# Performance work log

Measured on AMD Instinct MI355X. Metric: run time of the kernel, lower is better.

## Reference

```python
import jax, jax.numpy as jnp
import numpy as np

N_NODES = 100000
N_EDGES = 1600000
IN_DIM = 128
HID_DIM = 128


def gcn_conv(x, src, dst, W, b, n_nodes):
    """PyG GCNConv: out = D^{-1/2}(A+I)D^{-1/2} (x @ W) + b.
    src/dst already include self-loops."""
    h = x @ W  # [N, out_dim]
    deg = jnp.zeros((n_nodes,), dtype=h.dtype).at[dst].add(1.0)
    dis = jnp.where(deg > 0, jax.lax.rsqrt(jnp.maximum(deg, 1.0)), 0.0)
    norm = dis[src] * dis[dst]  # [E]
    msg = h[src] * norm[:, None]  # gather + scale, [E, out_dim]
    out = jax.ops.segment_sum(msg, dst, num_segments=n_nodes)
    return out + b


def setup_inputs() -> dict:
    key = jax.random.key(0)
    k1, k2, k3, k4, k5, k6 = jax.random.split(key, 6)
    x = jax.random.normal(k1, (N_NODES, IN_DIM), dtype=jnp.float32)
    edge_index = jax.random.randint(k2, (2, N_EDGES), 0, N_NODES, dtype=jnp.int32)
    s1 = 1.0 / np.sqrt(IN_DIM)
    s2 = 1.0 / np.sqrt(HID_DIM)
    W1 = jax.random.uniform(k3, (IN_DIM, HID_DIM), jnp.float32, -s1, s1)
    b1 = jax.random.uniform(k4, (HID_DIM,), jnp.float32, -s1, s1)
    W2 = jax.random.uniform(k5, (HID_DIM, HID_DIM), jnp.float32, -s2, s2)
    b2 = jax.random.uniform(k6, (HID_DIM,), jnp.float32, -s2, s2)
    return {"x": x, "edge_index": edge_index, "W1": W1, "b1": b1, "W2": W2, "b2": b2}


def reference(x, edge_index, W1, b1, W2, b2):
    n = x.shape[0]
    loops = jnp.arange(n, dtype=edge_index.dtype)
    src = jnp.concatenate([edge_index[0], loops])
    dst = jnp.concatenate([edge_index[1], loops])
    h = jax.nn.relu(gcn_conv(x, src, dst, W1, b1, n))
    h = jax.nn.relu(gcn_conv(h, src, dst, W2, b2, n))
    # global_mean_pool with batch = arange(N): each node is its own graph,
    # so the per-graph mean is the node feature itself.
    counts = jnp.ones((n, 1), dtype=h.dtype)
    pooled = jax.ops.segment_sum(h, jnp.arange(n), num_segments=n) / counts
    return pooled
```

## Files before the change

### kernel.cpp

```cpp
#include <hip/hip_runtime.h>
#include <hip/hip_fp16.h>
#include <stdint.h>
#include <stddef.h>

#define FEAT 128
#define BKT_SHIFT 8
#define TILE 4096
#define MAXB 400
#define CAP 4608

typedef _Float16 half8 __attribute__((ext_vector_type(8)));
typedef float f32x4 __attribute__((ext_vector_type(4)));


__global__ __launch_bounds__(256) void k_initB(int* __restrict__ cursorPad, int* __restrict__ allocCtr,
                                               const float* __restrict__ W1, const float* __restrict__ W2,
                                               _Float16* __restrict__ Wt1, _Float16* __restrict__ Wt2) {
  int i = blockIdx.x * 256 + threadIdx.x;
  if (i < MAXB * 16) cursorPad[i] = 0;
  if (i == 0) allocCtr[0] = 0;
  if (i < 32768) {
    int which = i >> 14, rem = i & 16383;
    int k = rem >> 7, nn = rem & 127;
    (which ? Wt2 : Wt1)[nn * 128 + k] = (_Float16)((which ? W2 : W1)[rem]);
  }
}


__global__ __launch_bounds__(256) void k_bscatter(const int* __restrict__ src, const int* __restrict__ dst,
                                                  int* __restrict__ cursorPad, int* __restrict__ pairs,
                                                  int E, int B) {
  __shared__ int h[MAXB];
  __shared__ int cur[MAXB];
  int t0 = blockIdx.x * TILE;
  int end = min(E, t0 + TILE);
  for (int i = threadIdx.x; i < B; i += 256) h[i] = 0;
  __syncthreads();
  if (end - t0 == TILE) {
    int d[16];
#pragma unroll
    for (int k = 0; k < 16; ++k) {
      d[k] = dst[t0 + threadIdx.x + k * 256];
      atomicAdd(&h[d[k] >> BKT_SHIFT], 1);
    }
    __syncthreads();
    for (int i = threadIdx.x; i < B; i += 256)
      cur[i] = h[i] ? atomicAdd(&cursorPad[i * 16], h[i]) : 0;
    __syncthreads();
#pragma unroll
    for (int k = 0; k < 16; ++k) {
      int e = t0 + threadIdx.x + k * 256;
      int b = d[k] >> BKT_SHIFT;
      int pos = atomicAdd(&cur[b], 1);
      if (pos < CAP) pairs[b * CAP + pos] = (src[e] << 8) | (d[k] & 255);
    }
  } else {
    for (int e = t0 + threadIdx.x; e < end; e += 256) atomicAdd(&h[dst[e] >> BKT_SHIFT], 1);
    __syncthreads();
    for (int i = threadIdx.x; i < B; i += 256)
      cur[i] = h[i] ? atomicAdd(&cursorPad[i * 16], h[i]) : 0;
    __syncthreads();
    for (int e = t0 + threadIdx.x; e < end; e += 256) {
      int dd = dst[e];
      int b = dd >> BKT_SHIFT;
      int pos = atomicAdd(&cur[b], 1);
      if (pos < CAP) pairs[b * CAP + pos] = (src[e] << 8) | (dd & 255);
    }
  }
}


__global__ __launch_bounds__(256) void k_csr(const int* __restrict__ pairs, const int* __restrict__ cursorPad,
                                             int* __restrict__ cnt, int* __restrict__ rowstart,
                                             float* __restrict__ dis, int* __restrict__ allocCtr,
                                             int* __restrict__ adj, int n) {
  __shared__ int deg[256];
  __shared__ int scan[256];
  __shared__ int curs[256];
  __shared__ int base;
  int b = blockIdx.x, t = threadIdx.x;
  int nodeBase = b << BKT_SHIFT;
  int e0 = b * CAP;
  int ecnt = min(cursorPad[b * 16], CAP);
  deg[t] = 0;
  __syncthreads();
  for (int i = t; i < ecnt; i += 256) atomicAdd(&deg[pairs[e0 + i] & 255], 1);
  __syncthreads();
  int d = deg[t];
  int padded = (d + 3) & ~3;
  scan[t] = padded;
  __syncthreads();
  for (int off = 1; off < 256; off <<= 1) {
    int x = scan[t];
    int y = (t >= off) ? scan[t - off] : 0;
    __syncthreads();
    scan[t] = x + y;
    __syncthreads();
  }
  int excl = scan[t] - padded;
  if (t == 255) base = atomicAdd(allocCtr, scan[t]);
  __syncthreads();
  int rs = base + excl;
  int node = nodeBase + t;
  if (node < n) {
    rowstart[node] = rs;
    cnt[node] = d;
    dis[node] = rsqrtf((float)(d + 1));
  }
  curs[t] = rs;
  __syncthreads();
  for (int i = t; i < ecnt; i += 256) {
    int pk = pairs[e0 + i];
    int pos = atomicAdd(&curs[pk & 255], 1);
    adj[pos] = pk >> 8;
  }
}


__global__ __launch_bounds__(256) void k_conv(const float* __restrict__ x, const float* __restrict__ dis,
                                              __half* __restrict__ t, int nElem) {
  int base = (blockIdx.x * 256 + threadIdx.x) * 4;
  if (base + 4 <= nElem) {
    float di = dis[base >> 7];
    float4 v = *(const float4*)(x + base);
    __half2* o = (__half2*)(t + base);
    o[0] = __floats2half2_rn(di * v.x, di * v.y);
    o[1] = __floats2half2_rn(di * v.z, di * v.w);
  }
}


__global__ __launch_bounds__(256) void k_agg(const __half* __restrict__ t, __half* __restrict__ z,
                                             const int* __restrict__ adj, const int* __restrict__ rowstart,
                                             const int* __restrict__ cnt, const float* __restrict__ dis, int n) {
  int node = blockIdx.x * 4 + (threadIdx.x >> 6);
  if (node >= n) return;
  int lane = threadIdx.x & 63;
  int rs = rowstart[node];
  int d = cnt[node];
  float di = dis[node];
  float2 a = __half22float2(((const __half2*)(t + (size_t)node * FEAT))[lane]);
  float ax = a.x, ay = a.y;
  int p = rs, e = rs + d;
#pragma unroll 2
  for (; p + 4 <= e; p += 4) {
    int4 j4 = *(const int4*)(adj + p);
    float2 h0 = __half22float2(((const __half2*)(t + (size_t)j4.x * FEAT))[lane]);
    float2 h1 = __half22float2(((const __half2*)(t + (size_t)j4.y * FEAT))[lane]);
    float2 h2 = __half22float2(((const __half2*)(t + (size_t)j4.z * FEAT))[lane]);
    float2 h3 = __half22float2(((const __half2*)(t + (size_t)j4.w * FEAT))[lane]);
    ax += (h0.x + h1.x) + (h2.x + h3.x);
    ay += (h0.y + h1.y) + (h2.y + h3.y);
  }
  for (; p < e; ++p) {
    int j = adj[p];
    float2 hv = __half22float2(((const __half2*)(t + (size_t)j * FEAT))[lane]);
    ax += hv.x; ay += hv.y;
  }
  ((__half2*)(z + (size_t)node * FEAT))[lane] = __floats2half2_rn(di * ax, di * ay);
}


template <bool OUT_HALF>
__global__ __launch_bounds__(256, 2) void k_gemm(const __half* __restrict__ Z,
                                                 const _Float16* __restrict__ Wt,
                                                 const float* __restrict__ bias,
                                                 const float* __restrict__ dis,
                                                 void* __restrict__ OutV, int n, int nwaves) {
  const int wid = (blockIdx.x * 256 + threadIdx.x) >> 6;
  const int lane = threadIdx.x & 63;
  const int lrow = lane & 15;
  const int lk8 = (lane >> 4) * 8;
  const int ngroups = (n + 15) >> 4;

  half8 bf[8][4];
#pragma unroll
  for (int c = 0; c < 8; ++c)
#pragma unroll
    for (int kk = 0; kk < 4; ++kk)
      bf[c][kk] = *(const half8*)(Wt + (size_t)(c * 16 + lrow) * 128 + kk * 32 + lk8);
  float bb[8];
#pragma unroll
  for (int c = 0; c < 8; ++c) bb[c] = bias[c * 16 + lrow];

  for (int g = wid; g < ngroups; g += nwaves) {
    int ar = g * 16 + lrow; if (ar >= n) ar = n - 1;
    const _Float16* arow = (const _Float16*)Z + (size_t)ar * 128 + lk8;
    half8 af[4];
#pragma unroll
    for (int kk = 0; kk < 4; ++kk) af[kk] = *(const half8*)(arow + kk * 32);
    f32x4 acc[8];
#pragma unroll
    for (int c = 0; c < 8; ++c) acc[c] = (f32x4){0.f, 0.f, 0.f, 0.f};
#pragma unroll
    for (int kk = 0; kk < 4; ++kk)
#pragma unroll
      for (int c = 0; c < 8; ++c)
        acc[c] = __builtin_amdgcn_mfma_f32_16x16x32_f16(af[kk], bf[c][kk], acc[c], 0, 0, 0);
    const int r0 = g * 16 + (lane >> 4) * 4;
#pragma unroll
    for (int r = 0; r < 4; ++r) {
      int row = r0 + r;
      if (row < n) {
        float sc = OUT_HALF ? dis[row] : 1.f;
#pragma unroll
        for (int c = 0; c < 8; ++c) {
          float vv = fmaxf(acc[c][r] + bb[c], 0.f);
          if (OUT_HALF) ((__half*)OutV)[(size_t)row * 128 + c * 16 + lrow] = __float2half_rn(sc * vv);
          else          ((float*)OutV)[(size_t)row * 128 + c * 16 + lrow] = vv;
        }
      }
    }
  }
}


extern "C" void kernel_launch(void* const* d_in, const int* in_sizes, int n_in,
                              void* d_out, int out_size, void* d_ws, size_t ws_size,
                              hipStream_t stream) {
  const float* x  = (const float*)d_in[0];
  const int*   ei = (const int*)d_in[1];
  const float* W1 = (const float*)d_in[2];
  const float* b1 = (const float*)d_in[3];
  const float* W2 = (const float*)d_in[4];
  const float* b2 = (const float*)d_in[5];
  float* out = (float*)d_out;

  const int n = in_sizes[0] / FEAT;
  const int E = in_sizes[1] / 2;
  const int B = (n + 255) >> BKT_SHIFT;
  const int* srcv = ei;
  const int* dstv = ei + E;

  uintptr_t p = (uintptr_t)d_ws;
  auto balloc = [&](size_t bytes) -> void* {
    void* r = (void*)p;
    p += (bytes + 255) & ~(size_t)255;
    return r;
  };
  __half*    T0   = (__half*)   balloc((size_t)n * FEAT * sizeof(__half));
  __half*    T1   = (__half*)   balloc((size_t)n * FEAT * sizeof(__half));
  __half*    Z16  = (__half*)   balloc((size_t)n * FEAT * sizeof(__half));
  _Float16*  Wt1  = (_Float16*) balloc(128 * 128 * sizeof(_Float16));
  _Float16*  Wt2  = (_Float16*) balloc(128 * 128 * sizeof(_Float16));
  int*   cnt      = (int*)  balloc((size_t)n * sizeof(int));
  int*   rowstart = (int*)  balloc((size_t)n * sizeof(int));
  float* dis      = (float*)balloc((size_t)n * sizeof(float));
  int*   allocCtr = (int*)  balloc(256);
  int*   cursorPad= (int*)  balloc((size_t)MAXB * 16 * sizeof(int));
  int*   pairs    = (int*)  balloc((size_t)MAXB * CAP * sizeof(int));
  int*   adj      = (int*)  balloc(((size_t)E + 4 * (size_t)n) * sizeof(int));
  (void)ws_size; (void)n_in; (void)out_size;

  const int nb  = (n + 255) / 256;
  const int tb  = (E + TILE - 1) / TILE;
  const int cb  = (n * FEAT / 4 + 255) / 256;

  k_initB   <<<nb, 256, 0, stream>>>(cursorPad, allocCtr, W1, W2, Wt1, Wt2);
  k_bscatter<<<tb, 256, 0, stream>>>(srcv, dstv, cursorPad, pairs, E, B);
  k_csr     <<<B, 256, 0, stream>>>(pairs, cursorPad, cnt, rowstart, dis, allocCtr, adj, n);
  k_conv    <<<cb, 256, 0, stream>>>(x, dis, T0, n * FEAT);

  const int ab = (n + 3) / 4;
  const int gemmBlocks = 512;
  const int nwaves = gemmBlocks * 4;

  k_agg        <<<ab, 256, 0, stream>>>(T0, Z16, adj, rowstart, cnt, dis, n);
  k_gemm<true> <<<gemmBlocks, 256, 0, stream>>>(Z16, Wt1, b1, dis, T1, n, nwaves);

  k_agg        <<<ab, 256, 0, stream>>>(T1, Z16, adj, rowstart, cnt, dis, n);
  k_gemm<false><<<gemmBlocks, 256, 0, stream>>>(Z16, Wt2, b2, dis, out, n, nwaves);
}
```

Measured before the change: 228.3 us.

## Fuse aggregation with GEMM via LDS tile and fold x conversion into CSR

The x-to-half scaling is folded into the CSR-building kernel, using the per-bucket degree values held in shared memory. Each layer's gather-aggregate is fused with the 128x128 MFMA GEMM: a block aggregates 16 nodes into a swizzled LDS tile, then its four waves each compute two output column groups. This removes the Z16 intermediate round trip and two kernel launches. In exchange, weight fragments are reloaded per block instead of staying in registers, and the CSR kernel now does extra streaming work in only about 400 blocks.

```diff
diff --git a/kernel.cpp b/kernel.cpp
--- a/kernel.cpp
+++ b/kernel.cpp
@@ -70,13 +70,15 @@
 }
 
 
-__global__ __launch_bounds__(256) void k_csr(const int* __restrict__ pairs, const int* __restrict__ cursorPad,
-                                             int* __restrict__ cnt, int* __restrict__ rowstart,
-                                             float* __restrict__ dis, int* __restrict__ allocCtr,
-                                             int* __restrict__ adj, int n) {
+__global__ __launch_bounds__(256) void k_csrc(const int* __restrict__ pairs, const int* __restrict__ cursorPad,
+                                              int* __restrict__ cnt, int* __restrict__ rowstart,
+                                              float* __restrict__ dis, int* __restrict__ allocCtr,
+                                              int* __restrict__ adj,
+                                              const float* __restrict__ x, __half* __restrict__ T0, int n) {
   __shared__ int deg[256];
   __shared__ int scan[256];
   __shared__ int curs[256];
+  __shared__ float disS[256];
   __shared__ int base;
   int b = blockIdx.x, t = threadIdx.x;
   int nodeBase = b << BKT_SHIFT;
@@ -91,10 +93,10 @@
   scan[t] = padded;
   __syncthreads();
   for (int off = 1; off < 256; off <<= 1) {
-    int x = scan[t];
+    int xg = scan[t];
     int y = (t >= off) ? scan[t - off] : 0;
     __syncthreads();
-    scan[t] = x + y;
+    scan[t] = xg + y;
     __syncthreads();
   }
   int excl = scan[t] - padded;
@@ -102,10 +104,12 @@
   __syncthreads();
   int rs = base + excl;
   int node = nodeBase + t;
+  float dv = rsqrtf((float)(d + 1));
+  disS[t] = dv;
   if (node < n) {
     rowstart[node] = rs;
     cnt[node] = d;
-    dis[node] = rsqrtf((float)(d + 1));
+    dis[node] = dv;
   }
   curs[t] = rs;
   __syncthreads();
@@ -114,101 +118,89 @@
     int pos = atomicAdd(&curs[pk & 255], 1);
     adj[pos] = pk >> 8;
   }
-}
-
-
-__global__ __launch_bounds__(256) void k_conv(const float* __restrict__ x, const float* __restrict__ dis,
-                                              __half* __restrict__ t, int nElem) {
-  int base = (blockIdx.x * 256 + threadIdx.x) * 4;
-  if (base + 4 <= nElem) {
-    float di = dis[base >> 7];
-    float4 v = *(const float4*)(x + base);
-    __half2* o = (__half2*)(t + base);
-    o[0] = __floats2half2_rn(di * v.x, di * v.y);
-    o[1] = __floats2half2_rn(di * v.z, di * v.w);
-  }
-}
-
-
-__global__ __launch_bounds__(256) void k_agg(const __half* __restrict__ t, __half* __restrict__ z,
-                                             const int* __restrict__ adj, const int* __restrict__ rowstart,
-                                             const int* __restrict__ cnt, const float* __restrict__ dis, int n) {
-  int node = blockIdx.x * 4 + (threadIdx.x >> 6);
-  if (node >= n) return;
-  int lane = threadIdx.x & 63;
-  int rs = rowstart[node];
-  int d = cnt[node];
-  float di = dis[node];
-  float2 a = __half22float2(((const __half2*)(t + (size_t)node * FEAT))[lane]);
-  float ax = a.x, ay = a.y;
-  int p = rs, e = rs + d;
+  for (int idx = t; idx < 256 * 32; idx += 256) {
+    int r = idx >> 5, c = idx & 31;
+    int nd = nodeBase + r;
+    if (nd >= n) continue;
+    float di = disS[r];
+    float4 v = ((const float4*)(x + (size_t)nd * FEAT))[c];
+    __half2 h0 = __floats2half2_rn(di * v.x, di * v.y);
+    __half2 h1 = __floats2half2_rn(di * v.z, di * v.w);
+    *(__half2*)(T0 + (size_t)nd * FEAT + c * 4)     = h0;
+    *(__half2*)(T0 + (size_t)nd * FEAT + c * 4 + 2) = h1;
+  }
+}
+
+
+template <bool OUT_HALF>
+__global__ __launch_bounds__(256) void k_fused(const __half* __restrict__ t, const _Float16* __restrict__ Wt,
+                                               const float* __restrict__ bias, const float* __restrict__ dis,
+                                               void* __restrict__ OutV,
+                                               const int* __restrict__ adj, const int* __restrict__ rowstart,
+                                               const int* __restrict__ cnt, int n) {
+  __shared__ __align__(16) char zb[16 * 256];
+  __shared__ float disL[16];
+  const int tid = threadIdx.x, w = tid >> 6, lane = tid & 63;
+  const int blockBase = blockIdx.x * 16;
+
+  for (int r = 0; r < 4; ++r) {
+    int local = w * 4 + r;
+    int node = blockBase + local;
+    float ax = 0.f, ay = 0.f, di = 0.f;
+    if (node < n) {
+      int rs = rowstart[node];
+      int d = cnt[node];
+      di = dis[node];
+      float2 a = __half22float2(((const __half2*)(t + (size_t)node * FEAT))[lane]);
+      ax = a.x; ay = a.y;
+      int p = rs, e = rs + d;
 #pragma unroll 2
-  for (; p + 4 <= e; p += 4) {
-    int4 j4 = *(const int4*)(adj + p);
-    float2 h0 = __half22float2(((const __half2*)(t + (size_t)j4.x * FEAT))[lane]);
-    float2 h1 = __half22float2(((const __half2*)(t + (size_t)j4.y * FEAT))[lane]);
-    float2 h2 = __half22float2(((const __half2*)(t + (size_t)j4.z * FEAT))[lane]);
-    float2 h3 = __half22float2(((const __half2*)(t + (size_t)j4.w * FEAT))[lane]);
-    ax += (h0.x + h1.x) + (h2.x + h3.x);
-    ay += (h0.y + h1.y) + (h2.y + h3.y);
-  }
-  for (; p < e; ++p) {
-    int j = adj[p];
-    float2 hv = __half22float2(((const __half2*)(t + (size_t)j * FEAT))[lane]);
-    ax += hv.x; ay += hv.y;
-  }
-  ((__half2*)(z + (size_t)node * FEAT))[lane] = __floats2half2_rn(di * ax, di * ay);
-}
-
-
-template <bool OUT_HALF>
-__global__ __launch_bounds__(256, 2) void k_gemm(const __half* __restrict__ Z,
-                                                 const _Float16* __restrict__ Wt,
-                                                 const float* __restrict__ bias,
-                                                 const float* __restrict__ dis,
-                                                 void* __restrict__ OutV, int n, int nwaves) {
-  const int wid = (blockIdx.x * 256 + threadIdx.x) >> 6;
-  const int lane = threadIdx.x & 63;
-  const int lrow = lane & 15;
-  const int lk8 = (lane >> 4) * 8;
-  const int ngroups = (n + 15) >> 4;
-
-  half8 bf[8][4];
-#pragma unroll
-  for (int c = 0; c < 8; ++c)
-#pragma unroll
-    for (int kk = 0; kk < 4; ++kk)
-      bf[c][kk] = *(const half8*)(Wt + (size_t)(c * 16 + lrow) * 128 + kk * 32 + lk8);
-  float bb[8];
-#pragma unroll
-  for (int c = 0; c < 8; ++c) bb[c] = bias[c * 16 + lrow];
-
-  for (int g = wid; g < ngroups; g += nwaves) {
-    int ar = g * 16 + lrow; if (ar >= n) ar = n - 1;
-    const _Float16* arow = (const _Float16*)Z + (size_t)ar * 128 + lk8;
-    half8 af[4];
-#pragma unroll
-    for (int kk = 0; kk < 4; ++kk) af[kk] = *(const half8*)(arow + kk * 32);
-    f32x4 acc[8];
-#pragma unroll
-    for (int c = 0; c < 8; ++c) acc[c] = (f32x4){0.f, 0.f, 0.f, 0.f};
-#pragma unroll
-    for (int kk = 0; kk < 4; ++kk)
-#pragma unroll
-      for (int c = 0; c < 8; ++c)
-        acc[c] = __builtin_amdgcn_mfma_f32_16x16x32_f16(af[kk], bf[c][kk], acc[c], 0, 0, 0);
-    const int r0 = g * 16 + (lane >> 4) * 4;
+      for (; p + 4 <= e; p += 4) {
+        int4 j4 = *(const int4*)(adj + p);
+        float2 h0 = __half22float2(((const __half2*)(t + (size_t)j4.x * FEAT))[lane]);
+        float2 h1 = __half22float2(((const __half2*)(t + (size_t)j4.y * FEAT))[lane]);
+        float2 h2 = __half22float2(((const __half2*)(t + (size_t)j4.z * FEAT))[lane]);
+        float2 h3 = __half22float2(((const __half2*)(t + (size_t)j4.w * FEAT))[lane]);
+        ax += (h0.x + h1.x) + (h2.x + h3.x);
+        ay += (h0.y + h1.y) + (h2.y + h3.y);
+      }
+      for (; p < e; ++p) {
+        int j = adj[p];
+        float2 hv = __half22float2(((const __half2*)(t + (size_t)j * FEAT))[lane]);
+        ax += hv.x; ay += hv.y;
+      }
+    }
+    if (lane == 0) disL[local] = di;
+    int boff = local * 256 + ((lane * 4) ^ ((local & 7) << 4));
+    *(__half2*)(zb + boff) = __floats2half2_rn(di * ax, di * ay);
+  }
+  __syncthreads();
+
+  const int lrow = lane & 15, g4 = lane >> 4;
+  half8 af[4];
+#pragma unroll
+  for (int kk = 0; kk < 4; ++kk) {
+    int cb = (kk * 64 + g4 * 16) ^ ((lrow & 7) << 4);
+    af[kk] = *(const half8*)(zb + lrow * 256 + cb);
+  }
+#pragma unroll
+  for (int c2 = 0; c2 < 2; ++c2) {
+    const int c = w * 2 + c2;
+    f32x4 acc = (f32x4){0.f, 0.f, 0.f, 0.f};
+#pragma unroll
+    for (int kk = 0; kk < 4; ++kk) {
+      half8 bf = *(const half8*)(Wt + (size_t)(c * 16 + lrow) * 128 + kk * 32 + g4 * 8);
+      acc = __builtin_amdgcn_mfma_f32_16x16x32_f16(af[kk], bf, acc, 0, 0, 0);
+    }
+    float bb = bias[c * 16 + lrow];
+    const int r0 = g4 * 4;
 #pragma unroll
     for (int r = 0; r < 4; ++r) {
-      int row = r0 + r;
+      int row = blockBase + r0 + r;
       if (row < n) {
-        float sc = OUT_HALF ? dis[row] : 1.f;
-#pragma unroll
-        for (int c = 0; c < 8; ++c) {
-          float vv = fmaxf(acc[c][r] + bb[c], 0.f);
-          if (OUT_HALF) ((__half*)OutV)[(size_t)row * 128 + c * 16 + lrow] = __float2half_rn(sc * vv);
-          else          ((float*)OutV)[(size_t)row * 128 + c * 16 + lrow] = vv;
-        }
+        float vv = fmaxf(acc[r] + bb, 0.f);
+        if (OUT_HALF) ((__half*)OutV)[(size_t)row * FEAT + c * 16 + lrow] = __float2half_rn(disL[r0 + r] * vv);
+        else          ((float*)OutV)[(size_t)row * FEAT + c * 16 + lrow] = vv;
       }
     }
   }
@@ -240,7 +232,6 @@
   };
   __half*    T0   = (__half*)   balloc((size_t)n * FEAT * sizeof(__half));
   __half*    T1   = (__half*)   balloc((size_t)n * FEAT * sizeof(__half));
-  __half*    Z16  = (__half*)   balloc((size_t)n * FEAT * sizeof(__half));
   _Float16*  Wt1  = (_Float16*) balloc(128 * 128 * sizeof(_Float16));
   _Float16*  Wt2  = (_Float16*) balloc(128 * 128 * sizeof(_Float16));
   int*   cnt      = (int*)  balloc((size_t)n * sizeof(int));
@@ -254,20 +245,12 @@
 
   const int nb  = (n + 255) / 256;
   const int tb  = (E + TILE - 1) / TILE;
-  const int cb  = (n * FEAT / 4 + 255) / 256;
+  const int fb  = (n + 15) / 16;
 
   k_initB   <<<nb, 256, 0, stream>>>(cursorPad, allocCtr, W1, W2, Wt1, Wt2);
   k_bscatter<<<tb, 256, 0, stream>>>(srcv, dstv, cursorPad, pairs, E, B);
-  k_csr     <<<B, 256, 0, stream>>>(pairs, cursorPad, cnt, rowstart, dis, allocCtr, adj, n);
-  k_conv    <<<cb, 256, 0, stream>>>(x, dis, T0, n * FEAT);
-
-  const int ab = (n + 3) / 4;
-  const int gemmBlocks = 512;
-  const int nwaves = gemmBlocks * 4;
-
-  k_agg        <<<ab, 256, 0, stream>>>(T0, Z16, adj, rowstart, cnt, dis, n);
-  k_gemm<true> <<<gemmBlocks, 256, 0, stream>>>(Z16, Wt1, b1, dis, T1, n, nwaves);
-
-  k_agg        <<<ab, 256, 0, stream>>>(T1, Z16, adj, rowstart, cnt, dis, n);
-  k_gemm<false><<<gemmBlocks, 256, 0, stream>>>(Z16, Wt2, b2, dis, out, n, nwaves);
-}
+  k_csrc    <<<B, 256, 0, stream>>>(pairs, cursorPad, cnt, rowstart, dis, allocCtr, adj, x, T0, n);
+
+  k_fused<true> <<<fb, 256, 0, stream>>>(T0, Wt1, b1, dis, T1, adj, rowstart, cnt, n);
+  k_fused<false><<<fb, 256, 0, stream>>>(T1, Wt2, b2, dis, out, adj, rowstart, cnt, n);
+}
```

After: 258.1 us. +13.0%, slower.

## Reorder GCN layers to transform-then-aggregate and fuse input conversion into GEMM

Applied to the files above, without the earlier changes.

Each layer now runs the 128x128 GEMM first, scaling by dis inside its epilogue, and then the neighbour aggregation, which applies the bias, ReLU and the output cast. This removes the separate fp32-to-fp16 conversion kernel, because the first GEMM reads x directly in fp32. The final layer writes fp32 output straight from the aggregation. The number of launches drops by one and the aggregation and GEMM bodies are redistributed, but fp16 rounding now happens at a different point in the computation.

```diff
diff --git a/kernel.cpp b/kernel.cpp
--- a/kernel.cpp
+++ b/kernel.cpp
@@ -117,28 +117,76 @@
 }
 
 
-__global__ __launch_bounds__(256) void k_conv(const float* __restrict__ x, const float* __restrict__ dis,
-                                              __half* __restrict__ t, int nElem) {
-  int base = (blockIdx.x * 256 + threadIdx.x) * 4;
-  if (base + 4 <= nElem) {
-    float di = dis[base >> 7];
-    float4 v = *(const float4*)(x + base);
-    __half2* o = (__half2*)(t + base);
-    o[0] = __floats2half2_rn(di * v.x, di * v.y);
-    o[1] = __floats2half2_rn(di * v.z, di * v.w);
-  }
-}
-
-
-__global__ __launch_bounds__(256) void k_agg(const __half* __restrict__ t, __half* __restrict__ z,
+template <bool A32>
+__global__ __launch_bounds__(256, 2) void k_gemm(const void* __restrict__ Av,
+                                                 const _Float16* __restrict__ Wt,
+                                                 const float* __restrict__ dis,
+                                                 __half* __restrict__ T, int n, int nwaves) {
+  const int wid = (blockIdx.x * 256 + threadIdx.x) >> 6;
+  const int lane = threadIdx.x & 63;
+  const int lrow = lane & 15;
+  const int lk8 = (lane >> 4) * 8;
+  const int ngroups = (n + 15) >> 4;
+
+  half8 bf[8][4];
+#pragma unroll
+  for (int c = 0; c < 8; ++c)
+#pragma unroll
+    for (int kk = 0; kk < 4; ++kk)
+      bf[c][kk] = *(const half8*)(Wt + (size_t)(c * 16 + lrow) * 128 + kk * 32 + lk8);
+
+  for (int g = wid; g < ngroups; g += nwaves) {
+    int ar = g * 16 + lrow; if (ar >= n) ar = n - 1;
+    half8 af[4];
+    if (A32) {
+      const float* arow = (const float*)Av + (size_t)ar * 128 + lk8;
+#pragma unroll
+      for (int kk = 0; kk < 4; ++kk) {
+        float4 v0 = *(const float4*)(arow + kk * 32);
+        float4 v1 = *(const float4*)(arow + kk * 32 + 4);
+        af[kk] = (half8){(_Float16)v0.x, (_Float16)v0.y, (_Float16)v0.z, (_Float16)v0.w,
+                         (_Float16)v1.x, (_Float16)v1.y, (_Float16)v1.z, (_Float16)v1.w};
+      }
+    } else {
+      const _Float16* arow = (const _Float16*)Av + (size_t)ar * 128 + lk8;
+#pragma unroll
+      for (int kk = 0; kk < 4; ++kk) af[kk] = *(const half8*)(arow + kk * 32);
+    }
+    f32x4 acc[8];
+#pragma unroll
+    for (int c = 0; c < 8; ++c) acc[c] = (f32x4){0.f, 0.f, 0.f, 0.f};
+#pragma unroll
+    for (int kk = 0; kk < 4; ++kk)
+#pragma unroll
+      for (int c = 0; c < 8; ++c)
+        acc[c] = __builtin_amdgcn_mfma_f32_16x16x32_f16(af[kk], bf[c][kk], acc[c], 0, 0, 0);
+    const int r0 = g * 16 + (lane >> 4) * 4;
+#pragma unroll
+    for (int r = 0; r < 4; ++r) {
+      int row = r0 + r;
+      if (row < n) {
+        float sc = dis[row];
+#pragma unroll
+        for (int c = 0; c < 8; ++c)
+          T[(size_t)row * 128 + c * 16 + lrow] = __float2half_rn(sc * acc[c][r]);
+      }
+    }
+  }
+}
+
+
+template <bool FINAL>
+__global__ __launch_bounds__(256) void k_agg(const __half* __restrict__ t, const float* __restrict__ bias,
                                              const int* __restrict__ adj, const int* __restrict__ rowstart,
-                                             const int* __restrict__ cnt, const float* __restrict__ dis, int n) {
+                                             const int* __restrict__ cnt, const float* __restrict__ dis,
+                                             void* __restrict__ outV, int n) {
   int node = blockIdx.x * 4 + (threadIdx.x >> 6);
   if (node >= n) return;
   int lane = threadIdx.x & 63;
   int rs = rowstart[node];
   int d = cnt[node];
   float di = dis[node];
+  float2 bb = ((const float2*)bias)[lane];
   float2 a = __half22float2(((const __half2*)(t + (size_t)node * FEAT))[lane]);
   float ax = a.x, ay = a.y;
   int p = rs, e = rs + d;
@@ -157,61 +205,10 @@
     float2 hv = __half22float2(((const __half2*)(t + (size_t)j * FEAT))[lane]);
     ax += hv.x; ay += hv.y;
   }
-  ((__half2*)(z + (size_t)node * FEAT))[lane] = __floats2half2_rn(di * ax, di * ay);
-}
-
-
-template <bool OUT_HALF>
-__global__ __launch_bounds__(256, 2) void k_gemm(const __half* __restrict__ Z,
-                                                 const _Float16* __restrict__ Wt,
-                                                 const float* __restrict__ bias,
-                                                 const float* __restrict__ dis,
-                                                 void* __restrict__ OutV, int n, int nwaves) {
-  const int wid = (blockIdx.x * 256 + threadIdx.x) >> 6;
-  const int lane = threadIdx.x & 63;
-  const int lrow = lane & 15;
-  const int lk8 = (lane >> 4) * 8;
-  const int ngroups = (n + 15) >> 4;
-
-  half8 bf[8][4];
-#pragma unroll
-  for (int c = 0; c < 8; ++c)
-#pragma unroll
-    for (int kk = 0; kk < 4; ++kk)
-      bf[c][kk] = *(const half8*)(Wt + (size_t)(c * 16 + lrow) * 128 + kk * 32 + lk8);
-  float bb[8];
-#pragma unroll
-  for (int c = 0; c < 8; ++c) bb[c] = bias[c * 16 + lrow];
-
-  for (int g = wid; g < ngroups; g += nwaves) {
-    int ar = g * 16 + lrow; if (ar >= n) ar = n - 1;
-    const _Float16* arow = (const _Float16*)Z + (size_t)ar * 128 + lk8;
-    half8 af[4];
-#pragma unroll
-    for (int kk = 0; kk < 4; ++kk) af[kk] = *(const half8*)(arow + kk * 32);
-    f32x4 acc[8];
-#pragma unroll
-    for (int c = 0; c < 8; ++c) acc[c] = (f32x4){0.f, 0.f, 0.f, 0.f};
-#pragma unroll
-    for (int kk = 0; kk < 4; ++kk)
-#pragma unroll
-      for (int c = 0; c < 8; ++c)
-        acc[c] = __builtin_amdgcn_mfma_f32_16x16x32_f16(af[kk], bf[c][kk], acc[c], 0, 0, 0);
-    const int r0 = g * 16 + (lane >> 4) * 4;
-#pragma unroll
-    for (int r = 0; r < 4; ++r) {
-      int row = r0 + r;
-      if (row < n) {
-        float sc = OUT_HALF ? dis[row] : 1.f;
-#pragma unroll
-        for (int c = 0; c < 8; ++c) {
-          float vv = fmaxf(acc[c][r] + bb[c], 0.f);
-          if (OUT_HALF) ((__half*)OutV)[(size_t)row * 128 + c * 16 + lrow] = __float2half_rn(sc * vv);
-          else          ((float*)OutV)[(size_t)row * 128 + c * 16 + lrow] = vv;
-        }
-      }
-    }
-  }
+  float vx = fmaxf(fmaf(di, ax, bb.x), 0.f);
+  float vy = fmaxf(fmaf(di, ay, bb.y), 0.f);
+  if (FINAL) ((float2*)((float*)outV + (size_t)node * FEAT))[lane] = make_float2(vx, vy);
+  else       ((__half2*)((__half*)outV + (size_t)node * FEAT))[lane] = __floats2half2_rn(vx, vy);
 }
 
 
@@ -238,9 +235,9 @@
     p += (bytes + 255) & ~(size_t)255;
     return r;
   };
-  __half*    T0   = (__half*)   balloc((size_t)n * FEAT * sizeof(__half));
   __half*    T1   = (__half*)   balloc((size_t)n * FEAT * sizeof(__half));
-  __half*    Z16  = (__half*)   balloc((size_t)n * FEAT * sizeof(__half));
+  __half*    H1   = (__half*)   balloc((size_t)n * FEAT * sizeof(__half));
+  __half*    T2   = (__half*)   balloc((size_t)n * FEAT * sizeof(__half));
   _Float16*  Wt1  = (_Float16*) balloc(128 * 128 * sizeof(_Float16));
   _Float16*  Wt2  = (_Float16*) balloc(128 * 128 * sizeof(_Float16));
   int*   cnt      = (int*)  balloc((size_t)n * sizeof(int));
@@ -254,20 +251,17 @@
 
   const int nb  = (n + 255) / 256;
   const int tb  = (E + TILE - 1) / TILE;
-  const int cb  = (n * FEAT / 4 + 255) / 256;
+  const int ab  = (n + 3) / 4;
+  const int gemmBlocks = 512;
+  const int nwaves = gemmBlocks * 4;
 
   k_initB   <<<nb, 256, 0, stream>>>(cursorPad, allocCtr, W1, W2, Wt1, Wt2);
   k_bscatter<<<tb, 256, 0, stream>>>(srcv, dstv, cursorPad, pairs, E, B);
   k_csr     <<<B, 256, 0, stream>>>(pairs, cursorPad, cnt, rowstart, dis, allocCtr, adj, n);
-  k_conv    <<<cb, 256, 0, stream>>>(x, dis, T0, n * FEAT);
-
-  const int ab = (n + 3) / 4;
-  const int gemmBlocks = 512;
-  const int nwaves = gemmBlocks * 4;
-
-  k_agg        <<<ab, 256, 0, stream>>>(T0, Z16, adj, rowstart, cnt, dis, n);
-  k_gemm<true> <<<gemmBlocks, 256, 0, stream>>>(Z16, Wt1, b1, dis, T1, n, nwaves);
-
-  k_agg        <<<ab, 256, 0, stream>>>(T1, Z16, adj, rowstart, cnt, dis, n);
-  k_gemm<false><<<gemmBlocks, 256, 0, stream>>>(Z16, Wt2, b2, dis, out, n, nwaves);
-}
+
+  k_gemm<true>  <<<gemmBlocks, 256, 0, stream>>>(x, Wt1, dis, T1, n, nwaves);
+  k_agg<false>  <<<ab, 256, 0, stream>>>(T1, b1, adj, rowstart, cnt, dis, H1, n);
+
+  k_gemm<false> <<<gemmBlocks, 256, 0, stream>>>(H1, Wt2, dis, T2, n, nwaves);
+  k_agg<true>   <<<ab, 256, 0, stream>>>(T2, b2, adj, rowstart, cnt, dis, out, n);
+}
```

New measurement: 223.5 us. 2.1% less time.
